# Kernel tuning notes

Measured on AMD Instinct MI355X. Metric: run time of the kernel, lower is better.

## Reference

```python
import jax, jax.numpy as jnp
import numpy as np

VOXEL_OFFSETS = jnp.array([-3.0, -3.0, -1.0], dtype=jnp.float32)
VOXEL_SIZE = 0.05


def setup_inputs() -> dict:
    key = jax.random.key(0)
    k1, k2 = jax.random.split(key)
    B, N = 4, 4096
    preds = jax.random.normal(k1, (B, N, 3), dtype=jnp.float32)
    gts = jax.random.normal(k2, (B, N, 3), dtype=jnp.float32)
    return {"preds": preds, "gts": gts}


def _chamfer(x, y):
    # x: [B, Nx, 3], y: [B, Ny, 3]
    # squared pairwise distances P[b, i, j] = ||x_bi - y_bj||^2
    xx = jnp.sum(x * x, axis=-1)  # [B, Nx]
    yy = jnp.sum(y * y, axis=-1)  # [B, Ny]
    zz = jnp.einsum('bnd,bmd->bnm', x, y)  # [B, Nx, Ny]
    P = xx[:, :, None] + yy[:, None, :] - 2.0 * zz
    dist1 = jnp.min(P, axis=2)  # nearest gt for each pred point, [B, Nx]
    dist2 = jnp.min(P, axis=1)  # nearest pred for each gt point, [B, Ny]
    return jnp.mean(dist1) + jnp.mean(dist2)


def _voxelize2(coord):
    # torch.div(coord - offsets, 0.05, rounding_mode='trunc') -> float grid coords
    return jnp.trunc((coord - VOXEL_OFFSETS) / VOXEL_SIZE)


def reference(preds, gts):
    # loss2 (point-space chamfer) is computed in the original but only logged
    loss2 = _chamfer(preds, gts)
    gts_voxel = _voxelize2(gts.astype(jnp.float32))
    preds_voxel = _voxelize2(preds.astype(jnp.float32))
    loss1 = _chamfer(preds_voxel, gts_voxel)
    # original forward returns loss1 only
    return loss1
```

## Files before the change

kernel.cpp:

```cpp
#include <hip/hip_runtime.h>
#include <math.h>


typedef float  f32x16 __attribute__((ext_vector_type(16)));
typedef short  bf16x8 __attribute__((ext_vector_type(8)));

constexpr int NPTS   = 4096;
constexpr int BLK    = 256;
constexpr int QPB    = 32;
constexpr int NTB    = NPTS / QPB;
constexpr int BATCH  = 4;
constexpr int NBLOCKS = 2 * BATCH * NTB;
constexpr int CHUNK  = 1024;
constexpr float FINF  = 3.402823466e38f;
constexpr float SCALE = 1.0f / 16384.0f;

__device__ __forceinline__ float vox(float c, float off) {
    return truncf((c + off) * 20.0f);
}
__device__ __forceinline__ unsigned bfbits(float v) {
    return __float_as_uint(v) >> 16;
}
__device__ __forceinline__ float min3f(float a, float b, float c) {
    return fminf(fminf(a, b), c);
}
__device__ __forceinline__ int4 packB(float x, float y, float z) {
    const float yy = fmaf(z, z, fmaf(y, y, x * x));
    const float hi = floorf(yy * 0.00390625f) * 256.0f;
    const float lo = yy - hi;
    return make_int4(
        (int)((bfbits(y) << 16) | bfbits(x)),
        (int)((bfbits(hi) << 16) | bfbits(z)),
        (int)(bfbits(lo)),
        0);
}

__global__ __launch_bounds__(BLK, 4) void chamfer_rows_kernel(
    const float* __restrict__ preds,
    const float* __restrict__ gts,
    float* __restrict__ partials)
{
    __shared__ int4  cfrag[CHUNK];
    __shared__ int4  qfrag[QPB];
    __shared__ float qxx[QPB];
    __shared__ float waveRow[4][QPB];

    const int t    = threadIdx.x;
    const int bid  = blockIdx.x;
    const int dir  = bid >> 9;
    const int rem  = bid & 511;
    const int b    = rem >> 7;
    const int tile = rem & 127;
    const int w    = t >> 6;
    const int lane = t & 63;
    const int col  = lane & 31;
    const bool lo_g = (lane < 32);

    const float* __restrict__ xb = (dir ? gts : preds) + (size_t)b * NPTS * 3;
    const float* __restrict__ yb = (dir ? preds : gts) + (size_t)b * NPTS * 3;

    constexpr unsigned ONE = 0x3F80u;

    if (t < QPB) {
        const int qi = tile * QPB + t;
        const float x = vox(xb[qi*3+0], 3.0f);
        const float y = vox(xb[qi*3+1], 3.0f);
        const float z = vox(xb[qi*3+2], 1.0f);
        qxx[t] = fmaf(z, z, fmaf(y, y, x * x));
        const float mx = -2.0f * x, my = -2.0f * y, mz = -2.0f * z;
        qfrag[t] = make_int4(
            (int)((bfbits(my) << 16) | bfbits(mx)),
            (int)((ONE << 16) | bfbits(mz)),
            (int)(ONE),
            0);
    }
    __syncthreads();

    bf16x8 afrag;
    {
        const int4 qv = qfrag[col];
        int4 ai = { lo_g ? qv.x : 0, lo_g ? qv.y : 0, lo_g ? qv.z : 0, 0 };
        afrag = __builtin_bit_cast(bf16x8, ai);
    }

    f32x16 rm;
    #pragma unroll
    for (int i = 0; i < 16; ++i) rm[i] = FINF;
    const f32x16 zero = {};

    const float4* __restrict__ yb4 = (const float4*)yb;

    #pragma unroll 1
    for (int cc = 0; cc < 4; ++cc) {
        if (cc) __syncthreads();
        {
            const int p0 = t * 4;
            const int fi = cc * 768 + t * 3;
            const float4 r0 = yb4[fi + 0];
            const float4 r1 = yb4[fi + 1];
            const float4 r2 = yb4[fi + 2];
            cfrag[p0+0] = packB(vox(r0.x,3.f), vox(r0.y,3.f), vox(r0.z,1.f));
            cfrag[p0+1] = packB(vox(r0.w,3.f), vox(r1.x,3.f), vox(r1.y,1.f));
            cfrag[p0+2] = packB(vox(r1.z,3.f), vox(r1.w,3.f), vox(r2.x,1.f));
            cfrag[p0+3] = packB(vox(r2.y,3.f), vox(r2.z,3.f), vox(r2.w,1.f));
        }
        __syncthreads();

        const int4* __restrict__ bbase = &cfrag[w * 256 + col];
        #pragma unroll
        for (int jp = 0; jp < 4; ++jp) {
            const bf16x8 bfa = __builtin_bit_cast(bf16x8, bbase[jp * 64]);
            const bf16x8 bfb = __builtin_bit_cast(bf16x8, bbase[jp * 64 + 32]);
            const f32x16 dA = __builtin_amdgcn_mfma_f32_32x32x16_bf16(
                afrag, bfa, zero, 0, 0, 0);
            const f32x16 dB = __builtin_amdgcn_mfma_f32_32x32x16_bf16(
                afrag, bfb, zero, 0, 0, 0);
            #pragma unroll
            for (int i = 0; i < 16; ++i)
                rm[i] = min3f(rm[i], dA[i], dB[i]);
        }
    }

    const int hi4 = (lane >> 5) * 4;
    #pragma unroll
    for (int i = 0; i < 16; ++i) {
        float v = rm[i];
        v = fminf(v, __shfl_xor(v, 1, 64));
        v = fminf(v, __shfl_xor(v, 2, 64));
        v = fminf(v, __shfl_xor(v, 4, 64));
        v = fminf(v, __shfl_xor(v, 8, 64));
        v = fminf(v, __shfl_xor(v, 16, 64));
        const int r = (i & 3) + 8 * (i >> 2) + hi4;
        if (col == 0) waveRow[w][r] = v + qxx[r];
    }
    __syncthreads();

    if (w == 0) {
        float s = 0.0f;
        if (lane < QPB) {
            s = fminf(fminf(waveRow[0][lane], waveRow[1][lane]),
                      fminf(waveRow[2][lane], waveRow[3][lane]));
        }
        #pragma unroll
        for (int o = 32; o >= 1; o >>= 1) s += __shfl_xor(s, o, 64);
        if (lane == 0) partials[bid] = s;
    }
}

__global__ __launch_bounds__(BLK) void chamfer_finish_kernel(
    const float* __restrict__ partials, float* __restrict__ out)
{
    __shared__ float s1[BLK];
    const int t = threadIdx.x;
    s1[t] = (partials[t] + partials[t + 256])
          + (partials[t + 512] + partials[t + 768]);
    __syncthreads();
    for (int k = 128; k > 0; k >>= 1) {
        if (t < k) s1[t] += s1[t + k];
        __syncthreads();
    }
    if (t == 0) out[0] = s1[0] * SCALE;
}

extern "C" void kernel_launch(void* const* d_in, const int* in_sizes, int n_in,
                              void* d_out, int out_size, void* d_ws, size_t ws_size,
                              hipStream_t stream)
{
    const float* preds = (const float*)d_in[0];
    const float* gts   = (const float*)d_in[1];
    float* out = (float*)d_out;
    float* partials = (float*)d_ws;

    chamfer_rows_kernel<<<NBLOCKS, BLK, 0, stream>>>(preds, gts, partials);
    chamfer_finish_kernel<<<1, BLK, 0, stream>>>(partials, out);
}
```

Baseline: 19.27 us.

## Double queries per block with two wave groups sharing staged candidate chunks

Result: faster. 17.51 us (-9.2%).

```diff
diff --git a/kernel.cpp b/kernel.cpp
--- a/kernel.cpp
+++ b/kernel.cpp
@@ -6,8 +6,8 @@
 typedef short  bf16x8 __attribute__((ext_vector_type(8)));
 
 constexpr int NPTS   = 4096;
-constexpr int BLK    = 256;
-constexpr int QPB    = 32;
+constexpr int BLK    = 512;
+constexpr int QPB    = 64;
 constexpr int NTB    = NPTS / QPB;
 constexpr int BATCH  = 4;
 constexpr int NBLOCKS = 2 * BATCH * NTB;
@@ -18,8 +18,10 @@
 __device__ __forceinline__ float vox(float c, float off) {
     return truncf((c + off) * 20.0f);
 }
-__device__ __forceinline__ unsigned bfbits(float v) {
-    return __float_as_uint(v) >> 16;
+__device__ __forceinline__ unsigned cvtpk(float lo, float hi) {
+    unsigned r;
+    asm("v_cvt_pk_bf16_f32 %0, %1, %2" : "=v"(r) : "v"(lo), "v"(hi));
+    return r;
 }
 __device__ __forceinline__ float min3f(float a, float b, float c) {
     return fminf(fminf(a, b), c);
@@ -28,11 +30,10 @@
     const float yy = fmaf(z, z, fmaf(y, y, x * x));
     const float hi = floorf(yy * 0.00390625f) * 256.0f;
     const float lo = yy - hi;
-    return make_int4(
-        (int)((bfbits(y) << 16) | bfbits(x)),
-        (int)((bfbits(hi) << 16) | bfbits(z)),
-        (int)(bfbits(lo)),
-        0);
+    return make_int4((int)cvtpk(x, y),
+                     (int)cvtpk(z, hi),
+                     (int)cvtpk(lo, 0.0f),
+                     0);
 }
 
 __global__ __launch_bounds__(BLK, 4) void chamfer_rows_kernel(
@@ -43,23 +44,23 @@
     __shared__ int4  cfrag[CHUNK];
     __shared__ int4  qfrag[QPB];
     __shared__ float qxx[QPB];
-    __shared__ float waveRow[4][QPB];
+    __shared__ float waveRow[8][32];
 
     const int t    = threadIdx.x;
     const int bid  = blockIdx.x;
-    const int dir  = bid >> 9;
-    const int rem  = bid & 511;
-    const int b    = rem >> 7;
-    const int tile = rem & 127;
+    const int dir  = bid >> 8;
+    const int rem  = bid & 255;
+    const int b    = rem >> 6;
+    const int tile = rem & 63;
     const int w    = t >> 6;
+    const int g    = w >> 2;
+    const int wsub = w & 3;
     const int lane = t & 63;
     const int col  = lane & 31;
     const bool lo_g = (lane < 32);
 
     const float* __restrict__ xb = (dir ? gts : preds) + (size_t)b * NPTS * 3;
     const float* __restrict__ yb = (dir ? preds : gts) + (size_t)b * NPTS * 3;
-
-    constexpr unsigned ONE = 0x3F80u;
 
     if (t < QPB) {
         const int qi = tile * QPB + t;
@@ -68,17 +69,16 @@
         const float z = vox(xb[qi*3+2], 1.0f);
         qxx[t] = fmaf(z, z, fmaf(y, y, x * x));
         const float mx = -2.0f * x, my = -2.0f * y, mz = -2.0f * z;
-        qfrag[t] = make_int4(
-            (int)((bfbits(my) << 16) | bfbits(mx)),
-            (int)((ONE << 16) | bfbits(mz)),
-            (int)(ONE),
-            0);
+        qfrag[t] = make_int4((int)cvtpk(mx, my),
+                             (int)cvtpk(mz, 1.0f),
+                             (int)cvtpk(1.0f, 0.0f),
+                             0);
     }
     __syncthreads();
 
     bf16x8 afrag;
     {
-        const int4 qv = qfrag[col];
+        const int4 qv = qfrag[g * 32 + col];
         int4 ai = { lo_g ? qv.x : 0, lo_g ? qv.y : 0, lo_g ? qv.z : 0, 0 };
         afrag = __builtin_bit_cast(bf16x8, ai);
     }
@@ -88,25 +88,23 @@
     for (int i = 0; i < 16; ++i) rm[i] = FINF;
     const f32x16 zero = {};
 
-    const float4* __restrict__ yb4 = (const float4*)yb;
+    const float2* __restrict__ yb2 = (const float2*)yb;
 
     #pragma unroll 1
     for (int cc = 0; cc < 4; ++cc) {
         if (cc) __syncthreads();
         {
-            const int p0 = t * 4;
-            const int fi = cc * 768 + t * 3;
-            const float4 r0 = yb4[fi + 0];
-            const float4 r1 = yb4[fi + 1];
-            const float4 r2 = yb4[fi + 2];
-            cfrag[p0+0] = packB(vox(r0.x,3.f), vox(r0.y,3.f), vox(r0.z,1.f));
-            cfrag[p0+1] = packB(vox(r0.w,3.f), vox(r1.x,3.f), vox(r1.y,1.f));
-            cfrag[p0+2] = packB(vox(r1.z,3.f), vox(r1.w,3.f), vox(r2.x,1.f));
-            cfrag[p0+3] = packB(vox(r2.y,3.f), vox(r2.z,3.f), vox(r2.w,1.f));
+            const int p0 = t * 2;
+            const int fi = cc * 1536 + t * 3;
+            const float2 r0 = yb2[fi + 0];
+            const float2 r1 = yb2[fi + 1];
+            const float2 r2 = yb2[fi + 2];
+            cfrag[p0+0] = packB(vox(r0.x,3.f), vox(r0.y,3.f), vox(r1.x,1.f));
+            cfrag[p0+1] = packB(vox(r1.y,3.f), vox(r2.x,3.f), vox(r2.y,1.f));
         }
         __syncthreads();
 
-        const int4* __restrict__ bbase = &cfrag[w * 256 + col];
+        const int4* __restrict__ bbase = &cfrag[wsub * 256 + col];
         #pragma unroll
         for (int jp = 0; jp < 4; ++jp) {
             const bf16x8 bfa = __builtin_bit_cast(bf16x8, bbase[jp * 64]);
@@ -131,26 +129,26 @@
         v = fminf(v, __shfl_xor(v, 8, 64));
         v = fminf(v, __shfl_xor(v, 16, 64));
         const int r = (i & 3) + 8 * (i >> 2) + hi4;
-        if (col == 0) waveRow[w][r] = v + qxx[r];
+        if (col == 0) waveRow[w][r] = v + qxx[g * 32 + r];
     }
     __syncthreads();
 
-    if (w == 0) {
+    if ((w & 3) == 0) {
         float s = 0.0f;
-        if (lane < QPB) {
-            s = fminf(fminf(waveRow[0][lane], waveRow[1][lane]),
-                      fminf(waveRow[2][lane], waveRow[3][lane]));
+        if (lane < 32) {
+            s = fminf(fminf(waveRow[w + 0][lane], waveRow[w + 1][lane]),
+                      fminf(waveRow[w + 2][lane], waveRow[w + 3][lane]));
         }
         #pragma unroll
         for (int o = 32; o >= 1; o >>= 1) s += __shfl_xor(s, o, 64);
-        if (lane == 0) partials[bid] = s;
+        if (lane == 0) partials[bid * 2 + g] = s;
     }
 }
 
-__global__ __launch_bounds__(BLK) void chamfer_finish_kernel(
+__global__ __launch_bounds__(256) void chamfer_finish_kernel(
     const float* __restrict__ partials, float* __restrict__ out)
 {
-    __shared__ float s1[BLK];
+    __shared__ float s1[256];
     const int t = threadIdx.x;
     s1[t] = (partials[t] + partials[t + 256])
           + (partials[t + 512] + partials[t + 768]);
@@ -172,5 +170,5 @@
     float* partials = (float*)d_ws;
 
     chamfer_rows_kernel<<<NBLOCKS, BLK, 0, stream>>>(preds, gts, partials);
-    chamfer_finish_kernel<<<1, BLK, 0, stream>>>(partials, out);
+    chamfer_finish_kernel<<<1, 256, 0, stream>>>(partials, out);
 }
```
